# Kernel tuning notes

Hardware: AMD Instinct MI355X
Metric: run time of the kernel (lower is better)

## Reference

```python
import jax, jax.numpy as jnp
import numpy as np

EPS = 1e-5
GROUPS = 8


def conv3x3(x, w, b):
    # x: [B,Cin,H,W], w: [Cout,Cin,3,3]
    y = jax.lax.conv_general_dilated(x, w, (1, 1), 'SAME',
                                     dimension_numbers=('NCHW', 'OIHW', 'NCHW'))
    return y + b[None, :, None, None]


def group_norm(x, scale, bias):
    B, C, H, W = x.shape
    xg = x.reshape(B, GROUPS, C // GROUPS, H, W)
    mu = jnp.mean(xg, axis=(2, 3, 4), keepdims=True)
    var = jnp.var(xg, axis=(2, 3, 4), keepdims=True)
    xn = ((xg - mu) * jax.lax.rsqrt(var + EPS)).reshape(B, C, H, W)
    return xn * scale[None, :, None, None] + bias[None, :, None, None]


def setup_inputs() -> dict:
    key = jax.random.key(0)
    ks = jax.random.split(key, 18)
    B, C, D, H, W = 8, 256, 128, 128, 128
    s = 0.02
    return {
        'current_feat': jax.random.normal(ks[0], (B, C, H, W), jnp.float32),
        'prev_hidden': jax.random.normal(ks[1], (B, D, H, W), jnp.float32),
        'conv1_w': jax.random.normal(ks[2], (D, C, 3, 3), jnp.float32) * s,
        'conv1_b': jnp.zeros((D,), jnp.float32),
        'gn_scale': jnp.ones((D,), jnp.float32),
        'gn_bias': jnp.zeros((D,), jnp.float32),
        'ce_w1': jax.random.normal(ks[3], (64, 4), jnp.float32) * 0.5,
        'ce_b1': jnp.zeros((64,), jnp.float32),
        'ce_w2': jax.random.normal(ks[4], (D, 64), jnp.float32) * 0.125,
        'ce_b2': jnp.zeros((D,), jnp.float32),
        'w_ih': jax.random.normal(ks[5], (3 * D, 3 * D), jnp.float32) * s,
        'b_ih': jnp.zeros((3 * D,), jnp.float32),
        'w_hh': jax.random.normal(ks[6], (3 * D, D), jnp.float32) * s,
        'b_hh': jnp.zeros((3 * D,), jnp.float32),
        'conv2_w': jax.random.normal(ks[7], (C, D, 3, 3), jnp.float32) * s,
        'conv2_b': jnp.zeros((C,), jnp.float32),
    }


def reference(current_feat, prev_hidden, conv1_w, conv1_b, gn_scale, gn_bias,
              ce_w1, ce_b1, ce_w2, ce_b2, w_ih, b_ih, w_hh, b_hh,
              conv2_w, conv2_b):
    B, C, H, W = current_feat.shape
    D = conv1_w.shape[0]

    # spatial_proj: conv -> GroupNorm(8) -> exact GELU
    spatial = jax.nn.gelu(group_norm(conv3x3(current_feat, conv1_w, conv1_b),
                                     gn_scale, gn_bias), approximate=False)

    # coordinate embedding (Linear(4,64) -> ReLU -> Linear(64,D))
    xc = jnp.broadcast_to(jnp.linspace(-1.0, 1.0, W)[None, None, :], (B, H, W))
    yc = jnp.broadcast_to(jnp.linspace(-1.0, 1.0, H)[None, :, None], (B, H, W))
    coord = jnp.stack([xc, yc, xc * H, yc * W], axis=-1)       # [B,H,W,4]
    ce = jax.nn.relu(coord @ ce_w1.T + ce_b1) @ ce_w2.T + ce_b2  # [B,H,W,D]
    coord_emb = jnp.transpose(ce, (0, 3, 1, 2))                 # [B,D,H,W]

    # batched GRUCell over all B*H*W positions (no spatial recurrence)
    gru_in = jnp.concatenate([spatial, coord_emb, prev_hidden], axis=1)  # [B,3D,H,W]
    Xf = jnp.transpose(gru_in, (0, 2, 3, 1)).reshape(-1, 3 * D)          # [N,3D]
    hf = jnp.transpose(prev_hidden, (0, 2, 3, 1)).reshape(-1, D)         # [N,D]
    gi = Xf @ w_ih.T + b_ih
    gh = hf @ w_hh.T + b_hh
    i_r, i_z, i_n = jnp.split(gi, 3, axis=-1)
    h_r, h_z, h_n = jnp.split(gh, 3, axis=-1)
    r = jax.nn.sigmoid(i_r + h_r)
    z = jax.nn.sigmoid(i_z + h_z)
    n = jnp.tanh(i_n + r * h_n)
    h_new = (1.0 - z) * n + z * hf                                       # [N,D]
    new_hidden = jnp.transpose(h_new.reshape(B, H, W, D), (0, 3, 1, 2))  # [B,D,H,W]

    # output_proj (Dropout2d inactive in eval) + residual
    output_feat = conv3x3(new_hidden, conv2_w, conv2_b) + current_feat
    return output_feat, new_hidden
```

## Files before the change

kernel.cpp:

```cpp
#include <hip/hip_runtime.h>
#include <math.h>

#define BH 8
#define HH 128
#define WW 128
#define HW 16384

typedef __attribute__((ext_vector_type(8))) short bf16x8;
typedef __attribute__((ext_vector_type(4))) float f32x4;

__device__ inline unsigned short f2bf(float f) {
    union { float f; unsigned u; } v; v.f = f;
    unsigned r = v.u + 0x7FFF + ((v.u >> 16) & 1);
    return (unsigned short)(r >> 16);
}
__device__ inline float bf2f(unsigned short u) {
    union { unsigned u; float f; } v; v.u = (unsigned)u << 16;
    return v.f;
}

typedef const __attribute__((address_space(1))) void* gptr_t;
typedef __attribute__((address_space(3))) void* lptr_t;
__device__ inline void gload_lds16(const void* g, void* l) {
    __builtin_amdgcn_global_load_lds((gptr_t)g, (lptr_t)l, 16, 0, 0);
}

__global__ __launch_bounds__(256) void transpose_cast(
        const float* __restrict__ in, unsigned short* __restrict__ out, int C) {
    __shared__ float T[32][65];
    int tid = threadIdx.x;
    int pb = blockIdx.x * 64, cb = blockIdx.y * 32, b = blockIdx.z;
    #pragma unroll
    for (int j = 0; j < 8; ++j) {
        int idx = tid + j * 256;
        int c = idx >> 6, p = idx & 63;
        T[c][p] = in[((size_t)(b * C + cb + c)) * HW + pb + p];
    }
    __syncthreads();
    #pragma unroll
    for (int j = 0; j < 8; ++j) {
        int idx = tid + j * 256;
        int p = idx >> 5, c = idx & 31;
        out[((size_t)(b * (C / 32) + blockIdx.y) * HW + pb + p) * 32 + c] = f2bf(T[c][p]);
    }
}

__global__ __launch_bounds__(256) void repack_weights(
        const float* __restrict__ w1, const float* __restrict__ w2,
        const float* __restrict__ wih, const float* __restrict__ whh,
        unsigned short* __restrict__ w1t, unsigned short* __restrict__ w2t,
        unsigned short* __restrict__ wg) {
    int i = blockIdx.x * 256 + threadIdx.x;
    if (i < 294912) {
        int e = i & 7, l15 = (i >> 3) & 15, quad = (i >> 7) & 3;
        int f16 = (i >> 9) & 7, cc = (i >> 12) & 7, t = i >> 15;
        int d = f16 * 16 + l15, c = cc * 32 + quad * 8 + e;
        w1t[i] = f2bf(w1[((size_t)(d * 256 + c)) * 9 + t]);
    }
    if (i < 294912) {
        int e = i & 7, l15 = (i >> 3) & 15, quad = (i >> 7) & 3;
        int f16 = (i >> 9) & 15, cc = (i >> 13) & 3, t = i >> 15;
        int co = f16 * 16 + l15, ci = cc * 32 + quad * 8 + e;
        w2t[i] = f2bf(w2[((size_t)(co * 128 + ci)) * 9 + t]);
    }
    if (i < 196608) {
        int e = i & 7, l15 = (i >> 3) & 15, quad = (i >> 7) & 3;
        int f16 = (i >> 9) & 31, ck = i >> 14;
        int m = f16 * 16 + l15, k = ck * 32 + quad * 8 + e;
        float v = 0.0f;
        if (m < 384) {
            if (k < 128)       v = wih[(size_t)m * 384 + k];
            else if (k < 256)  v = wih[(size_t)m * 384 + 256 + (k - 128)];
            else               v = (m < 256) ? whh[(size_t)m * 128 + (k - 256)] : 0.0f;
        } else {
            v = (k >= 256) ? whh[(size_t)(m - 128) * 128 + (k - 256)] : 0.0f;
        }
        wg[i] = f2bf(v);
    }
}

__global__ __launch_bounds__(256) void prep_ce(
        const float* __restrict__ w2, const float* __restrict__ b2,
        const float* __restrict__ wih,
        float* __restrict__ M, float* __restrict__ cebias) {
    int i = blockIdx.x * 256 + threadIdx.x;
    if (i < 24576) {
        int j = i / 384, m = i - j * 384;
        float acc = 0.0f;
        for (int d = 0; d < 128; ++d)
            acc = fmaf(w2[(size_t)d * 64 + j], wih[(size_t)m * 384 + 128 + d], acc);
        M[i] = acc;
    } else if (i < 24960) {
        int m = i - 24576;
        float acc = 0.0f;
        for (int d = 0; d < 128; ++d)
            acc = fmaf(b2[d], wih[(size_t)m * 384 + 128 + d], acc);
        cebias[m] = acc;
    }
}

__global__ __launch_bounds__(384) void ce_g_kernel(
        const float* __restrict__ w1, const float* __restrict__ b1,
        const float* __restrict__ M, const float* __restrict__ cebias,
        float* __restrict__ ce_g) {
    __shared__ float h1[16][64];
    int m = threadIdx.x;
    int pos0 = blockIdx.x * 16;
    for (int e = m; e < 1024; e += 384) {
        int p = e >> 6, j = e & 63;
        int pos = pos0 + p;
        int hh = pos >> 7, wp = pos & 127;
        float xc = -1.0f + 2.0f * (float)wp / 127.0f;
        float yc = -1.0f + 2.0f * (float)hh / 127.0f;
        float a = xc * w1[j*4+0] + yc * w1[j*4+1]
                + xc * 128.0f * w1[j*4+2] + yc * 128.0f * w1[j*4+3] + b1[j];
        h1[p][j] = fmaxf(a, 0.0f);
    }
    __syncthreads();
    float acc[16];
    float cb = cebias[m];
    #pragma unroll
    for (int p = 0; p < 16; ++p) acc[p] = cb;
    for (int j = 0; j < 64; ++j) {
        float Mv = M[(size_t)j * 384 + m];
        #pragma unroll
        for (int p = 0; p < 16; ++p)
            acc[p] = fmaf(h1[p][j], Mv, acc[p]);
    }
    #pragma unroll
    for (int p = 0; p < 16; ++p)
        ce_g[(size_t)(pos0 + p) * 384 + m] = acc[p];
}

template<int CIN, int COUT, bool CONV1>
__global__ __launch_bounds__(256, 3) void conv_mfma(
        const unsigned short* __restrict__ xt,
        const unsigned short* __restrict__ wt,
        const float* __restrict__ bias,
        float* __restrict__ stats_acc,
        const float* __restrict__ resid,
        unsigned short* __restrict__ y_bf,
        float* __restrict__ y_f32,
        const unsigned short* __restrict__ zbuf) {
    constexpr int NCC  = CIN / 32;
    constexpr int NT   = 3 * NCC;
    constexpr int NF16 = COUT / 16;
    __shared__ unsigned short Ash[2][130 * 32];

    const int tid = threadIdx.x;
    const int h = ((blockIdx.x & 7) << 4) + (blockIdx.x >> 3);
    const int b = blockIdx.y;
    const int cobase = blockIdx.z * 128;
    const int lane = tid & 63, wave = tid >> 6;
    const int wn = (wave & 1) * 64, wd = (wave >> 1) * 64;
    const int l15 = lane & 15, quad = lane >> 4;

    f32x4 acc[4][4];
    #pragma unroll
    for (int i = 0; i < 4; ++i)
        #pragma unroll
        for (int j = 0; j < 4; ++j)
            acc[i][j] = (f32x4){0.f, 0.f, 0.f, 0.f};

    auto stageA = [&](int buf, int t) {
        const int kh = t / NCC, cc = t - kh * NCC;
        const int r = h + kh - 1;
        const bool oob = ((unsigned)r >= (unsigned)HH);
        const char* abase = oob ? (const char*)zbuf
            : (const char*)(xt + ((size_t)(b * NCC + cc) * HW + r * WW) * 32);
        #pragma unroll
        for (int j = 0; j < 2; ++j) {
            const int ob = 64 + (tid + j * 256) * 16;
            const int row = ob >> 6, cb = ob & 63;
            const int sel = (row >> 1) & 3;
            const char* src = oob ? abase + cb
                : abase + (size_t)(row - 1) * 64 + (cb ^ (sel << 4));
            gload_lds16(src, (char*)Ash[buf] + 64 + (wave * 64 + j * 256) * 16);
        }
    };

    if (tid < 16) {
        int buf = tid >> 3, hi = (tid >> 2) & 1, q = tid & 3;
        *(f32x4*)((char*)Ash[buf] + (hi ? 129 * 64 : 0) + q * 16) =
            (f32x4){0.f, 0.f, 0.f, 0.f};
    }
    stageA(0, 0);
    __syncthreads();

    int curb = 0;
    for (int t = 0; t < NT; ++t) {
        const int kh = t / NCC, cc = t - kh * NCC;
        bf16x8 wreg[3][4];
        #pragma unroll
        for (int kw = 0; kw < 3; ++kw)
            #pragma unroll
            for (int fd = 0; fd < 4; ++fd) {
                const int f16 = (cobase >> 4) + (wd >> 4) + fd;
                wreg[kw][fd] = *(const bf16x8*)(wt +
                    (((size_t)(kh * 3 + kw) * NCC + cc) * NF16 + f16) * 512 + lane * 8);
            }
        if (t + 1 < NT) stageA(curb ^ 1, t + 1);
        #pragma unroll
        for (int kw = 0; kw < 3; ++kw) {
            bf16x8 a[4];
            #pragma unroll
            for (int fn = 0; fn < 4; ++fn) {
                int ra = wn + fn * 16 + l15 + kw;
                a[fn] = *(const bf16x8*)&Ash[curb][ra * 32 +
                            (quad * 8 ^ (((ra >> 1) & 3) << 3))];
            }
            #pragma unroll
            for (int fn = 0; fn < 4; ++fn)
                #pragma unroll
                for (int fd = 0; fd < 4; ++fd)
                    acc[fn][fd] = __builtin_amdgcn_mfma_f32_16x16x32_bf16(
                        a[fn], wreg[kw][fd], acc[fn][fd], 0, 0, 0);
        }
        __syncthreads();
        curb ^= 1;
    }

    if (CONV1) {
        float gsum[4] = {0.f,0.f,0.f,0.f}, gss[4] = {0.f,0.f,0.f,0.f};
        #pragma unroll
        for (int fd = 0; fd < 4; ++fd) {
            int d = wd + fd * 16 + l15;
            float bv = bias[d];
            #pragma unroll
            for (int fn = 0; fn < 4; ++fn) {
                #pragma unroll
                for (int reg = 0; reg < 4; ++reg) {
                    int n = wn + fn * 16 + quad * 4 + reg;
                    float v = acc[fn][fd][reg] + bv;
                    y_bf[((size_t)(b * 4 + (d >> 5)) * HW + h * WW + n) * 32 + (d & 31)]
                        = f2bf(v);
                    gsum[fd] += v; gss[fd] += v * v;
                }
            }
        }
        #pragma unroll
        for (int fd = 0; fd < 4; ++fd) {
            float s = gsum[fd], q = gss[fd];
            for (int o = 32; o > 0; o >>= 1) {
                s += __shfl_down(s, o);
                q += __shfl_down(q, o);
            }
            if (lane == 0) {
                int g = (wd >> 4) + fd;
                atomicAdd(&stats_acc[(b * 8 + g) * 2], s);
                atomicAdd(&stats_acc[(b * 8 + g) * 2 + 1], q);
            }
        }
    } else {
        #pragma unroll
        for (int fd = 0; fd < 4; ++fd) {
            int co = cobase + wd + fd * 16 + l15;
            float bv = bias[co];
            #pragma unroll
            for (int fn = 0; fn < 4; ++fn) {
                int n0 = wn + fn * 16 + quad * 4;
                size_t ofs = ((size_t)(b * 256 + co)) * HW + h * WW + n0;
                float4 rs = *(const float4*)(resid + ofs);
                float4 o;
                o.x = acc[fn][fd][0] + bv + rs.x;
                o.y = acc[fn][fd][1] + bv + rs.y;
                o.z = acc[fn][fd][2] + bv + rs.z;
                o.w = acc[fn][fd][3] + bv + rs.w;
                *(float4*)(y_f32 + ofs) = o;
            }
        }
    }
}

__global__ void gn_finalize(float* stats) {
    int t = threadIdx.x;
    if (t < 64) {
        float s = stats[t*2], q = stats[t*2+1];
        const float inv = 1.0f / 262144.0f;
        float mean = s * inv;
        float var = q * inv - mean * mean;
        stats[t*2] = mean;
        stats[t*2+1] = rsqrtf(var + 1e-5f);
    }
}

__global__ __launch_bounds__(256) void gn_gelu(
        unsigned short* __restrict__ y, const float* __restrict__ stats,
        const float* __restrict__ scale, const float* __restrict__ bias) {
    size_t i = (size_t)blockIdx.x * 256 + threadIdx.x;
    size_t e = i * 4;
    int c32 = (int)(e & 31);
    int cc = (int)((e >> 19) & 3);
    int b = (int)(e >> 21);
    int d = cc * 32 + c32;
    int g = b * 8 + (d >> 4);
    float mean = stats[g * 2], rstd = stats[g * 2 + 1];
    ushort4 v = *(ushort4*)&y[e];
    unsigned short vs[4] = {v.x, v.y, v.z, v.w};
    #pragma unroll
    for (int j = 0; j < 4; ++j) {
        float a = rstd * scale[d + j];
        float c = bias[d + j] - mean * a;
        float t = bf2f(vs[j]) * a + c;
        vs[j] = f2bf(0.5f * t * (1.0f + erff(t * 0.70710678118654752f)));
    }
    ushort4 o = {vs[0], vs[1], vs[2], vs[3]};
    *(ushort4*)&y[e] = o;
}

__global__ __launch_bounds__(256, 4) void gru_gemm(
        const unsigned short* __restrict__ sp_t,
        const unsigned short* __restrict__ ph_t,
        const unsigned short* __restrict__ wg,
        unsigned short* __restrict__ G) {
    __shared__ unsigned short Xs[2][128 * 32];
    const int tid = threadIdx.x;
    const int nt = blockIdx.x, mt = blockIdx.y;
    const size_t p0 = (size_t)nt * 128;
    const int b4 = (nt >> 7) * 4;
    const int hw0 = (int)(p0 & (HW - 1));
    const int lane = tid & 63, wave = tid >> 6;
    const int wn = (wave & 1) * 64, wm = (wave >> 1) * 64;
    const int l15 = lane & 15, quad = lane >> 4;

    f32x4 acc[4][4];
    #pragma unroll
    for (int i = 0; i < 4; ++i)
        #pragma unroll
        for (int j = 0; j < 4; ++j)
            acc[i][j] = (f32x4){0.f, 0.f, 0.f, 0.f};

    auto stageX = [&](int buf, int ck) {
        const int cc = ck & 3;
        const unsigned short* srcbuf = (ck < 4) ? sp_t : ph_t;
        const char* xb = (const char*)(srcbuf + ((size_t)(b4 + cc) * HW + hw0) * 32);
        #pragma unroll
        for (int j = 0; j < 2; ++j) {
            const int ob = (tid + j * 256) * 16;
            const int row = ob >> 6, cb = ob & 63;
            const int sel = (row >> 1) & 3;
            gload_lds16(xb + (size_t)row * 64 + (cb ^ (sel << 4)),
                        (char*)Xs[buf] + (wave * 64 + j * 256) * 16);
        }
    };

    stageX(0, 0);
    __syncthreads();
    int curb = 0;
    for (int ck = 0; ck < 12; ++ck) {
        bf16x8 wreg[4];
        #pragma unroll
        for (int fm = 0; fm < 4; ++fm) {
            const int f16 = mt * 8 + (wm >> 4) + fm;
            wreg[fm] = *(const bf16x8*)(wg + ((size_t)(ck * 32 + f16)) * 512 + lane * 8);
        }
        if (ck + 1 < 12) stageX(curb ^ 1, ck + 1);
        bf16x8 a[4];
        #pragma unroll
        for (int fn = 0; fn < 4; ++fn) {
            int row = wn + fn * 16 + l15;
            a[fn] = *(const bf16x8*)&Xs[curb][row * 32 +
                        (quad * 8 ^ (((row >> 1) & 3) << 3))];
        }
        #pragma unroll
        for (int fn = 0; fn < 4; ++fn)
            #pragma unroll
            for (int fm = 0; fm < 4; ++fm)
                acc[fn][fm] = __builtin_amdgcn_mfma_f32_16x16x32_bf16(
                    a[fn], wreg[fm], acc[fn][fm], 0, 0, 0);
        __syncthreads();
        curb ^= 1;
    }
    #pragma unroll
    for (int fm = 0; fm < 4; ++fm) {
        int m = mt * 128 + wm + fm * 16 + l15;
        #pragma unroll
        for (int fn = 0; fn < 4; ++fn)
            #pragma unroll
            for (int reg = 0; reg < 4; ++reg) {
                int n = wn + fn * 16 + quad * 4 + reg;
                G[(p0 + n) * 512 + m] = f2bf(acc[fn][fm][reg]);
            }
    }
}

__global__ __launch_bounds__(256) void gru_gate(
        const unsigned short* __restrict__ G,
        const float* __restrict__ ce_g,
        const float* __restrict__ b_ih, const float* __restrict__ b_hh,
        const float* __restrict__ prev_f32,
        float* __restrict__ new_hidden, unsigned short* __restrict__ hn_t) {
    __shared__ float T[128][65];
    const int tid = threadIdx.x;
    const size_t p0 = (size_t)blockIdx.x * 64;
    const int b = (int)(p0 >> 14);
    const int hw0 = (int)(p0 & (HW - 1));
    const int d = tid & 127;
    const float br  = b_ih[d]       + b_hh[d];
    const float bz  = b_ih[128 + d] + b_hh[128 + d];
    const float bin = b_ih[256 + d];
    const float bhn = b_hh[256 + d];
    for (int j = 0; j < 32; ++j) {
        int pp = (tid >> 7) + j * 2;
        size_t gbase = (p0 + pp) * 512;
        size_t cbase = (size_t)(hw0 + pp) * 384;
        float rl = bf2f(G[gbase + d])       + ce_g[cbase + d]       + br;
        float zl = bf2f(G[gbase + 128 + d]) + ce_g[cbase + 128 + d] + bz;
        float il = bf2f(G[gbase + 256 + d]) + ce_g[cbase + 256 + d] + bin;
        float hl = bf2f(G[gbase + 384 + d]) + bhn;
        float r = 1.0f / (1.0f + expf(-rl));
        float z = 1.0f / (1.0f + expf(-zl));
        float n = tanhf(il + r * hl);
        float hp = prev_f32[((size_t)(b * 128 + d)) * HW + hw0 + pp];
        float hn = (1.0f - z) * n + z * hp;
        T[d][pp] = hn;
        hn_t[((size_t)(b * 4 + (d >> 5)) * HW + hw0 + pp) * 32 + (d & 31)] = f2bf(hn);
    }
    __syncthreads();
    #pragma unroll
    for (int j = 0; j < 8; ++j) {
        int idx = tid + j * 256;
        int d2 = idx >> 4, pp4 = (idx & 15) * 4;
        float4 v = { T[d2][pp4], T[d2][pp4+1], T[d2][pp4+2], T[d2][pp4+3] };
        *(float4*)&new_hidden[((size_t)(b * 128 + d2)) * HW + hw0 + pp4] = v;
    }
}

extern "C" void kernel_launch(void* const* d_in, const int* in_sizes, int n_in,
                              void* d_out, int out_size, void* d_ws, size_t ws_size,
                              hipStream_t stream) {
    const float* current_feat = (const float*)d_in[0];
    const float* prev_hidden  = (const float*)d_in[1];
    const float* conv1_w = (const float*)d_in[2];
    const float* conv1_b = (const float*)d_in[3];
    const float* gn_scale = (const float*)d_in[4];
    const float* gn_bias  = (const float*)d_in[5];
    const float* ce_w1 = (const float*)d_in[6];
    const float* ce_b1 = (const float*)d_in[7];
    const float* ce_w2 = (const float*)d_in[8];
    const float* ce_b2 = (const float*)d_in[9];
    const float* w_ih = (const float*)d_in[10];
    const float* b_ih = (const float*)d_in[11];
    const float* w_hh = (const float*)d_in[12];
    const float* b_hh = (const float*)d_in[13];
    const float* conv2_w = (const float*)d_in[14];
    const float* conv2_b = (const float*)d_in[15];

    char* ws = (char*)d_ws;
    unsigned short* cf_t = (unsigned short*)(ws);
    unsigned short* ph_t = (unsigned short*)(ws + 67108864);
    unsigned short* sp_t = (unsigned short*)(ws + 100663296);
    unsigned short* w1t  = (unsigned short*)(ws + 134217728);
    unsigned short* w2t  = (unsigned short*)(ws + 134807552);
    unsigned short* wg   = (unsigned short*)(ws + 135397376);
    float* Mmat          = (float*)(ws + 135790592);
    float* cebias        = (float*)(ws + 135888896);
    float* stats         = (float*)(ws + 135890432);
    unsigned short* zbuf = (unsigned short*)(ws + 135890944);
    unsigned short* hn_t = cf_t;
    float* ce_g          = (float*)(ws + 33554432);
    unsigned short* G    = (unsigned short*)d_out;
    float* out_feat      = (float*)d_out;
    float* new_hidden    = (float*)d_out + 33554432;

    hipMemsetAsync(stats, 0, 512, stream);
    hipMemsetAsync(zbuf, 0, 256, stream);
    hipLaunchKernelGGL(repack_weights, dim3(1152), dim3(256), 0, stream,
                       conv1_w, conv2_w, w_ih, w_hh, w1t, w2t, wg);
    hipLaunchKernelGGL(prep_ce, dim3(98), dim3(256), 0, stream,
                       ce_w2, ce_b2, w_ih, Mmat, cebias);
    hipLaunchKernelGGL(transpose_cast, dim3(256, 8, 8), dim3(256), 0, stream,
                       current_feat, cf_t, 256);
    hipLaunchKernelGGL(transpose_cast, dim3(256, 4, 8), dim3(256), 0, stream,
                       prev_hidden, ph_t, 128);
    hipLaunchKernelGGL((conv_mfma<256, 128, true>), dim3(128, 8, 1), dim3(256), 0, stream,
                       cf_t, w1t, conv1_b, stats, nullptr, sp_t, nullptr, zbuf);
    hipLaunchKernelGGL(ce_g_kernel, dim3(1024), dim3(384), 0, stream,
                       ce_w1, ce_b1, Mmat, cebias, ce_g);
    hipLaunchKernelGGL(gn_finalize, dim3(1), dim3(64), 0, stream, stats);
    hipLaunchKernelGGL(gn_gelu, dim3(16384), dim3(256), 0, stream,
                       sp_t, stats, gn_scale, gn_bias);
    hipLaunchKernelGGL(gru_gemm, dim3(1024, 4), dim3(256), 0, stream,
                       sp_t, ph_t, wg, G);
    hipLaunchKernelGGL(gru_gate, dim3(2048), dim3(256), 0, stream,
                       G, ce_g, b_ih, b_hh, prev_hidden, new_hidden, hn_t);
    hipLaunchKernelGGL((conv_mfma<128, 256, false>), dim3(128, 8, 2), dim3(256), 0, stream,
                       hn_t, w2t, conv2_b, nullptr, current_feat, nullptr, out_feat, zbuf);
}
```

Before: 1.008 ms.

## Compute two output rows per conv block to reuse weight registers

Each conv block now computes two output image rows instead of one. It stages both input row strips into a larger LDS buffer and reuses each set of loaded weight fragments across both rows, which halves weight global loads per output and halves the grid size. The weight load for the next tile is also moved after the MFMA loop so it overlaps the barrier. This doubles accumulator registers, so the launch-bounds occupancy hint drops from 3 to 2 blocks per SM. It also raises LDS use and may spill or lower latency hiding.

```diff
diff --git a/kernel.cpp b/kernel.cpp
--- a/kernel.cpp
+++ b/kernel.cpp
@@ -133,7 +133,7 @@
 }
 
 template<int CIN, int COUT, bool CONV1>
-__global__ __launch_bounds__(256, 3) void conv_mfma(
+__global__ __launch_bounds__(256, 2) void conv_mfma(
         const unsigned short* __restrict__ xt,
         const unsigned short* __restrict__ wt,
         const float* __restrict__ bias,
@@ -145,52 +145,50 @@
     constexpr int NCC  = CIN / 32;
     constexpr int NT   = 3 * NCC;
     constexpr int NF16 = COUT / 16;
-    __shared__ unsigned short Ash[2][130 * 32];
+    __shared__ unsigned short Ash[2][259 * 32];
 
     const int tid = threadIdx.x;
-    const int h = ((blockIdx.x & 7) << 4) + (blockIdx.x >> 3);
+    const int hp = ((blockIdx.x & 7) << 3) + (blockIdx.x >> 3);
+    const int h0 = hp * 2;
     const int b = blockIdx.y;
     const int cobase = blockIdx.z * 128;
     const int lane = tid & 63, wave = tid >> 6;
     const int wn = (wave & 1) * 64, wd = (wave >> 1) * 64;
     const int l15 = lane & 15, quad = lane >> 4;
 
-    f32x4 acc[4][4];
-    #pragma unroll
-    for (int i = 0; i < 4; ++i)
-        #pragma unroll
-        for (int j = 0; j < 4; ++j)
-            acc[i][j] = (f32x4){0.f, 0.f, 0.f, 0.f};
+    f32x4 acc[2][4][4];
+    #pragma unroll
+    for (int r = 0; r < 2; ++r)
+        #pragma unroll
+        for (int i = 0; i < 4; ++i)
+            #pragma unroll
+            for (int j = 0; j < 4; ++j)
+                acc[r][i][j] = (f32x4){0.f, 0.f, 0.f, 0.f};
 
     auto stageA = [&](int buf, int t) {
         const int kh = t / NCC, cc = t - kh * NCC;
-        const int r = h + kh - 1;
-        const bool oob = ((unsigned)r >= (unsigned)HH);
-        const char* abase = oob ? (const char*)zbuf
-            : (const char*)(xt + ((size_t)(b * NCC + cc) * HW + r * WW) * 32);
-        #pragma unroll
-        for (int j = 0; j < 2; ++j) {
-            const int ob = 64 + (tid + j * 256) * 16;
-            const int row = ob >> 6, cb = ob & 63;
-            const int sel = (row >> 1) & 3;
-            const char* src = oob ? abase + cb
-                : abase + (size_t)(row - 1) * 64 + (cb ^ (sel << 4));
-            gload_lds16(src, (char*)Ash[buf] + 64 + (wave * 64 + j * 256) * 16);
+        #pragma unroll
+        for (int ri = 0; ri < 2; ++ri) {
+            const int r = h0 + kh - 1 + ri;
+            const bool oob = ((unsigned)r >= (unsigned)HH);
+            const char* abase = oob ? (const char*)zbuf
+                : (const char*)(xt + ((size_t)(b * NCC + cc) * HW + r * WW) * 32);
+            #pragma unroll
+            for (int j = 0; j < 2; ++j) {
+                const int ob = 64 + (tid + j * 256) * 16;
+                const int row = ob >> 6, cb = ob & 63;
+                const int sel = (row >> 1) & 3;
+                const char* src = oob ? abase + cb
+                    : abase + (size_t)(row - 1) * 64 + (cb ^ (sel << 4));
+                gload_lds16(src, (char*)Ash[buf] + ri * 8256 + 64 +
+                                 (wave * 64 + j * 256) * 16);
+            }
         }
     };
 
-    if (tid < 16) {
-        int buf = tid >> 3, hi = (tid >> 2) & 1, q = tid & 3;
-        *(f32x4*)((char*)Ash[buf] + (hi ? 129 * 64 : 0) + q * 16) =
-            (f32x4){0.f, 0.f, 0.f, 0.f};
-    }
-    stageA(0, 0);
-    __syncthreads();
-
-    int curb = 0;
-    for (int t = 0; t < NT; ++t) {
+    bf16x8 wreg[3][4];
+    auto loadW = [&](int t) {
         const int kh = t / NCC, cc = t - kh * NCC;
-        bf16x8 wreg[3][4];
         #pragma unroll
         for (int kw = 0; kw < 3; ++kw)
             #pragma unroll
@@ -199,23 +197,39 @@
                 wreg[kw][fd] = *(const bf16x8*)(wt +
                     (((size_t)(kh * 3 + kw) * NCC + cc) * NF16 + f16) * 512 + lane * 8);
             }
+    };
+
+    if (tid < 24) {
+        int buf = tid / 12, s = (tid % 12) >> 2, q = tid & 3;
+        *(f32x4*)((char*)Ash[buf] + s * 8256 + q * 16) = (f32x4){0.f,0.f,0.f,0.f};
+    }
+    stageA(0, 0);
+    loadW(0);
+    __syncthreads();
+
+    int curb = 0;
+    for (int t = 0; t < NT; ++t) {
         if (t + 1 < NT) stageA(curb ^ 1, t + 1);
         #pragma unroll
         for (int kw = 0; kw < 3; ++kw) {
-            bf16x8 a[4];
-            #pragma unroll
-            for (int fn = 0; fn < 4; ++fn) {
-                int ra = wn + fn * 16 + l15 + kw;
-                a[fn] = *(const bf16x8*)&Ash[curb][ra * 32 +
-                            (quad * 8 ^ (((ra >> 1) & 3) << 3))];
-            }
-            #pragma unroll
-            for (int fn = 0; fn < 4; ++fn)
+            #pragma unroll
+            for (int ri = 0; ri < 2; ++ri) {
+                bf16x8 a[4];
                 #pragma unroll
-                for (int fd = 0; fd < 4; ++fd)
-                    acc[fn][fd] = __builtin_amdgcn_mfma_f32_16x16x32_bf16(
-                        a[fn], wreg[kw][fd], acc[fn][fd], 0, 0, 0);
-        }
+                for (int fn = 0; fn < 4; ++fn) {
+                    int ra = wn + fn * 16 + l15 + kw;
+                    a[fn] = *(const bf16x8*)&Ash[curb][ri * 4128 + ra * 32 +
+                                (quad * 8 ^ (((ra >> 1) & 3) << 3))];
+                }
+                #pragma unroll
+                for (int fn = 0; fn < 4; ++fn)
+                    #pragma unroll
+                    for (int fd = 0; fd < 4; ++fd)
+                        acc[ri][fn][fd] = __builtin_amdgcn_mfma_f32_16x16x32_bf16(
+                            a[fn], wreg[kw][fd], acc[ri][fn][fd], 0, 0, 0);
+            }
+        }
+        if (t + 1 < NT) loadW(t + 1);
         __syncthreads();
         curb ^= 1;
     }
@@ -227,14 +241,17 @@
             int d = wd + fd * 16 + l15;
             float bv = bias[d];
             #pragma unroll
-            for (int fn = 0; fn < 4; ++fn) {
+            for (int ri = 0; ri < 2; ++ri) {
                 #pragma unroll
-                for (int reg = 0; reg < 4; ++reg) {
-                    int n = wn + fn * 16 + quad * 4 + reg;
-                    float v = acc[fn][fd][reg] + bv;
-                    y_bf[((size_t)(b * 4 + (d >> 5)) * HW + h * WW + n) * 32 + (d & 31)]
-                        = f2bf(v);
-                    gsum[fd] += v; gss[fd] += v * v;
+                for (int fn = 0; fn < 4; ++fn) {
+                    #pragma unroll
+                    for (int reg = 0; reg < 4; ++reg) {
+                        int n = wn + fn * 16 + quad * 4 + reg;
+                        float v = acc[ri][fn][fd][reg] + bv;
+                        y_bf[((size_t)(b * 4 + (d >> 5)) * HW + (h0 + ri) * WW + n) * 32
+                             + (d & 31)] = f2bf(v);
+                        gsum[fd] += v; gss[fd] += v * v;
+                    }
                 }
             }
         }
@@ -257,16 +274,19 @@
             int co = cobase + wd + fd * 16 + l15;
             float bv = bias[co];
             #pragma unroll
-            for (int fn = 0; fn < 4; ++fn) {
-                int n0 = wn + fn * 16 + quad * 4;
-                size_t ofs = ((size_t)(b * 256 + co)) * HW + h * WW + n0;
-                float4 rs = *(const float4*)(resid + ofs);
-                float4 o;
-                o.x = acc[fn][fd][0] + bv + rs.x;
-                o.y = acc[fn][fd][1] + bv + rs.y;
-                o.z = acc[fn][fd][2] + bv + rs.z;
-                o.w = acc[fn][fd][3] + bv + rs.w;
-                *(float4*)(y_f32 + ofs) = o;
+            for (int ri = 0; ri < 2; ++ri) {
+                #pragma unroll
+                for (int fn = 0; fn < 4; ++fn) {
+                    int n0 = wn + fn * 16 + quad * 4;
+                    size_t ofs = ((size_t)(b * 256 + co)) * HW + (h0 + ri) * WW + n0;
+                    float4 rs = *(const float4*)(resid + ofs);
+                    float4 o;
+                    o.x = acc[ri][fn][fd][0] + bv + rs.x;
+                    o.y = acc[ri][fn][fd][1] + bv + rs.y;
+                    o.z = acc[ri][fn][fd][2] + bv + rs.z;
+                    o.w = acc[ri][fn][fd][3] + bv + rs.w;
+                    *(float4*)(y_f32 + ofs) = o;
+                }
             }
         }
     }
@@ -473,7 +493,7 @@
                        current_feat, cf_t, 256);
     hipLaunchKernelGGL(transpose_cast, dim3(256, 4, 8), dim3(256), 0, stream,
                        prev_hidden, ph_t, 128);
-    hipLaunchKernelGGL((conv_mfma<256, 128, true>), dim3(128, 8, 1), dim3(256), 0, stream,
+    hipLaunchKernelGGL((conv_mfma<256, 128, true>), dim3(64, 8, 1), dim3(256), 0, stream,
                        cf_t, w1t, conv1_b, stats, nullptr, sp_t, nullptr, zbuf);
     hipLaunchKernelGGL(ce_g_kernel, dim3(1024), dim3(384), 0, stream,
                        ce_w1, ce_b1, Mmat, cebias, ce_g);
@@ -484,6 +504,6 @@
                        sp_t, ph_t, wg, G);
     hipLaunchKernelGGL(gru_gate, dim3(2048), dim3(256), 0, stream,
                        G, ce_g, b_ih, b_hh, prev_hidden, new_hidden, hn_t);
-    hipLaunchKernelGGL((conv_mfma<128, 256, false>), dim3(128, 8, 2), dim3(256), 0, stream,
+    hipLaunchKernelGGL((conv_mfma<128, 256, false>), dim3(64, 8, 2), dim3(256), 0, stream,
                        hn_t, w2t, conv2_b, nullptr, current_feat, nullptr, out_feat, zbuf);
 }
```

New measurement: 907.6 us. 1.11x faster.
